# Kernel tuning notes

Measured on AMD Instinct MI355X. Metric: run time of the kernel, lower is better.

The kernel has to match this reference:

```python
import jax, jax.numpy as jnp
import numpy as np


def _gcn_conv(x, W, b, row, col, norm, n_nodes):
    # x: [N, Fin]; W: [Fin, Fout]. PyG GCNConv: linear -> normalized gather/scatter-add -> +bias
    h = x @ W                                   # [N, Fout]
    msgs = h[row] * norm[:, None]               # [E+N, Fout] gather + scale
    out = jax.ops.segment_sum(msgs, col, num_segments=n_nodes)  # scatter-add
    return out + b


def _gcn_norm(edge_index, n_nodes):
    # add self-loops, then sym-normalize: deg^{-1/2}[row] * deg^{-1/2}[col]
    loops = jnp.arange(n_nodes, dtype=edge_index.dtype)
    row = jnp.concatenate([edge_index[0], loops])
    col = jnp.concatenate([edge_index[1], loops])
    ones = jnp.ones(row.shape[0], dtype=jnp.float32)
    deg = jax.ops.segment_sum(ones, col, num_segments=n_nodes)
    dinv = jnp.where(deg > 0, jax.lax.rsqrt(deg), 0.0)
    norm = dinv[row] * dinv[col]
    return row, col, norm


def setup_inputs() -> dict:
    key = jax.random.key(0)
    k1, k2, k3, k4 = jax.random.split(key, 4)
    N, E, F, H, C = 100000, 1600000, 256, 128, 40
    x = jax.random.normal(k1, (N, F), dtype=jnp.float32)
    edge_index = jax.random.randint(k2, (2, E), 0, N, dtype=jnp.int64)
    W1 = jax.random.normal(k3, (F, H), dtype=jnp.float32) * (1.0 / np.sqrt(F))
    b1 = jnp.zeros((H,), dtype=jnp.float32)
    W2 = jax.random.normal(k4, (H, C), dtype=jnp.float32) * (1.0 / np.sqrt(H))
    b2 = jnp.zeros((C,), dtype=jnp.float32)
    return {"x": x, "edge_index": edge_index, "W1": W1, "b1": b1, "W2": W2, "b2": b2}


def reference(x, edge_index, W1, b1, W2, b2):
    n_nodes = x.shape[0]
    row, col, norm = _gcn_norm(edge_index, n_nodes)
    h = _gcn_conv(x, W1, b1, row, col, norm, n_nodes)
    h = jax.nn.relu(h)
    # F.dropout in eval mode is identity (reference run deterministically)
    h = _gcn_conv(h, W2, b2, row, col, norm, n_nodes)
    return jax.nn.log_softmax(h, axis=1)
```

## Files before the change

### kernel.cpp

```cpp
#include <hip/hip_runtime.h>
#include <hip/hip_bf16.h>
#include <math.h>
#include <stdint.h>

typedef unsigned short u16;
typedef unsigned int u32;
typedef __attribute__((ext_vector_type(8))) short short8;
typedef __attribute__((ext_vector_type(4))) float f32x4;
typedef __attribute__((ext_vector_type(2))) float f32x2;

#define BN 256
#define NBMAX 400
#define EPB 4096
#define ST1 160
#define ST2 192

__device__ __forceinline__ u16 bfbits(float f) {
    __hip_bfloat16 h = __float2bfloat16(f);
    return *reinterpret_cast<u16*>(&h);
}
__device__ __forceinline__ float bflo(u32 v) { return __uint_as_float(v << 16); }
__device__ __forceinline__ float bfhi(u32 v) { return __uint_as_float(v & 0xffff0000u); }

template <bool HI>
__device__ __forceinline__ f32x2 fp8pair(u32 v) {
#if __has_builtin(__builtin_amdgcn_cvt_pk_f32_fp8)
    return __builtin_amdgcn_cvt_pk_f32_fp8(v, HI);
#else
    f32x2 r;
    r.x = __builtin_amdgcn_cvt_f32_fp8(v, HI ? 2 : 0);
    r.y = __builtin_amdgcn_cvt_f32_fp8(v, HI ? 3 : 1);
    return r;
#endif
}

__global__ __launch_bounds__(256) void k_cnt(const int* __restrict__ col,
                                             int* __restrict__ gcnt, int E, int n, int nb) {
    __shared__ int sh[NBMAX];
    const int t = threadIdx.x;
    for (int i = t; i < nb; i += 256) sh[i] = 0;
    __syncthreads();
    const int base = blockIdx.x * EPB;
#pragma unroll
    for (int j = 0; j < 16; ++j) {
        int e = base + j * 256 + t;
        if (e < E) {
            unsigned c = (unsigned)col[e];
            if (c < (unsigned)n) atomicAdd(&sh[c >> 8], 1);
        }
    }
    __syncthreads();
    for (int i = t; i < nb; i += 256)
        if (sh[i]) atomicAdd(&gcnt[i], sh[i]);
}

__global__ __launch_bounds__(512) void k_bscan(const int* __restrict__ gcnt,
                                               int* __restrict__ ebase, int* __restrict__ cursor,
                                               int* __restrict__ off, int nb, int n) {
    __shared__ int sh[512];
    const int t = threadIdx.x;
    int v = (t < nb) ? gcnt[t] : 0;
    sh[t] = v;
    __syncthreads();
    for (int d = 1; d < 512; d <<= 1) {
        int x = (t >= d) ? sh[t - d] : 0;
        __syncthreads();
        sh[t] += x;
        __syncthreads();
    }
    if (t < nb) {
        int excl = sh[t] - v;
        ebase[t] = excl;
        cursor[t] = excl;
    }
    if (t == 0) {
        ebase[nb] = sh[511];
        off[n] = sh[511] + n;
    }
}

__global__ __launch_bounds__(256) void k_scat(const int* __restrict__ ei,
                                              int* __restrict__ cursor,
                                              u32* __restrict__ staging, int E, int n, int nb) {
    __shared__ int cnt[NBMAX];
    __shared__ int cbase[NBMAX];
    const int t = threadIdx.x;
    for (int i = t; i < nb; i += 256) cnt[i] = 0;
    __syncthreads();
    const int base = blockIdx.x * EPB;
    int rr[16], cc[16], rk[16];
#pragma unroll
    for (int j = 0; j < 16; ++j) {
        int e = base + j * 256 + t;
        cc[j] = -1;
        if (e < E) {
            unsigned r = (unsigned)ei[e], c = (unsigned)ei[E + e];
            if (r < (unsigned)n && c < (unsigned)n) {
                rr[j] = (int)r;
                cc[j] = (int)c;
                rk[j] = atomicAdd(&cnt[c >> 8], 1);
            }
        }
    }
    __syncthreads();
    for (int i = t; i < nb; i += 256)
        if (cnt[i]) cbase[i] = atomicAdd(&cursor[i], cnt[i]);
    __syncthreads();
#pragma unroll
    for (int j = 0; j < 16; ++j) {
        if (cc[j] >= 0) {
            int b = cc[j] >> 8;
            staging[cbase[b] + rk[j]] = (u32)rr[j] | ((u32)(cc[j] & (BN - 1)) << 17);
        }
    }
}

__global__ __launch_bounds__(256) void k_build(const u32* __restrict__ staging,
                                               const int* __restrict__ ebase,
                                               int* __restrict__ csrs, int* __restrict__ off,
                                               float* __restrict__ dinv, int n) {
    __shared__ int sh[256];
    __shared__ int cur[256];
    const int t = threadIdx.x;
    const int b = blockIdx.x;
    const int e0 = ebase[b], e1 = ebase[b + 1];
    const int node0 = b * BN;
    const int nn = min(BN, n - node0);
    sh[t] = 0;
    __syncthreads();
    for (int i = e0 + t; i < e1; i += 256)
        atomicAdd(&sh[staging[i] >> 17], 1);
    __syncthreads();
    const int mycnt = sh[t];
    const int myval = (t < nn) ? mycnt + 1 : 0;
    sh[t] = myval;
    __syncthreads();
    for (int d = 1; d < 256; d <<= 1) {
        int x = (t >= d) ? sh[t - d] : 0;
        __syncthreads();
        sh[t] += x;
        __syncthreads();
    }
    const int excl = sh[t] - myval;
    const int csrbase = e0 + node0;
    if (t < nn) {
        int node = node0 + t;
        int o = csrbase + excl;
        off[node] = o;
        dinv[node] = rsqrtf((float)(mycnt + 1));
        csrs[o] = node;
        cur[t] = o + 1;
    }
    __syncthreads();
    for (int i = e0 + t; i < e1; i += 256) {
        u32 v = staging[i];
        int p = atomicAdd(&cur[v >> 17], 1);
        csrs[p] = (int)(v & 0x1FFFF);
    }
}

__global__ void k_w1bf(const float* __restrict__ w1, short* __restrict__ w1bf) {
    int i = blockIdx.x * 256 + threadIdx.x;
    int e = i & 7, l = (i >> 3) & 63, kt = (i >> 9) & 7, ct = i >> 12;
    int k = kt * 32 + (l >> 4) * 8 + e;
    int c = ct * 16 + (l & 15);
    w1bf[i] = (short)bfbits(w1[(size_t)k * 128 + c]);
}

__device__ __forceinline__ int sigma128(int col) {
    int a = col >> 6, c = (col >> 4) & 3, lr = col & 15;
    return (a << 6) + (lr << 2) + c;
}
__global__ void k_prep(const float* __restrict__ b1, const float* __restrict__ w2,
                       float* __restrict__ b1p, float* __restrict__ w2p) {
    int i = blockIdx.x * 256 + threadIdx.x;
    if (i < 128) b1p[sigma128(i)] = b1[i];
    int j = i - 128;
    if (j >= 0 && j < 128 * 40) {
        int col = j / 40, jj = j - col * 40;
        w2p[sigma128(col) * 40 + jj] = w2[j];
    }
}

__global__ __launch_bounds__(256) void k_gemm1(const float* __restrict__ x,
                                               const short* __restrict__ w1bf,
                                               u32* __restrict__ hbf8, int n) {
    const int tid = threadIdx.x;
    const int wv = tid >> 6, l = tid & 63;
    const int mrow = wv >> 1, mcol = wv & 1;
    const int lr = l & 15, kg = l >> 4;
    const int n0 = blockIdx.x * 64;

    const float* xp[2];
#pragma unroll
    for (int m = 0; m < 2; ++m) {
        int row = n0 + 32 * mrow + 16 * m + lr;
        if (row > n - 1) row = n - 1;
        xp[m] = x + (size_t)row * 256 + kg * 8;
    }
    const short* bbase = w1bf + ((size_t)(4 * mcol) * 8) * 64 * 8 + (size_t)l * 8;

    float4 xv[2][8][2];
#pragma unroll
    for (int kt = 0; kt < 8; ++kt)
#pragma unroll
        for (int m = 0; m < 2; ++m) {
            xv[m][kt][0] = *(const float4*)(xp[m] + kt * 32);
            xv[m][kt][1] = *(const float4*)(xp[m] + kt * 32 + 4);
        }

    f32x4 zero = {0.f, 0.f, 0.f, 0.f};
    f32x4 acc[2][4];
#pragma unroll
    for (int m = 0; m < 2; ++m)
#pragma unroll
        for (int c = 0; c < 4; ++c) acc[m][c] = zero;

#pragma unroll
    for (int kt = 0; kt < 8; ++kt) {
        short8 af[2];
#pragma unroll
        for (int m = 0; m < 2; ++m) {
            float4 u = xv[m][kt][0];
            float4 v = xv[m][kt][1];
            short8 a;
            a[0] = (short)bfbits(u.x);
            a[1] = (short)bfbits(u.y);
            a[2] = (short)bfbits(u.z);
            a[3] = (short)bfbits(u.w);
            a[4] = (short)bfbits(v.x);
            a[5] = (short)bfbits(v.y);
            a[6] = (short)bfbits(v.z);
            a[7] = (short)bfbits(v.w);
            af[m] = a;
        }
#pragma unroll
        for (int c = 0; c < 4; ++c) {
            short8 bfrag = *(const short8*)(bbase + ((size_t)(c * 8 + kt) * 64) * 8);
#pragma unroll
            for (int m = 0; m < 2; ++m)
                acc[m][c] = __builtin_amdgcn_mfma_f32_16x16x32_bf16(af[m], bfrag,
                                                                    acc[m][c], 0, 0, 0);
        }
    }

#pragma unroll
    for (int m = 0; m < 2; ++m) {
        int rbase = n0 + 32 * mrow + 16 * m + kg * 4;
#pragma unroll
        for (int r = 0; r < 4; ++r) {
            int row = rbase + r;
            if (row < n) {
                int w = __builtin_amdgcn_cvt_pk_fp8_f32(acc[m][0][r], acc[m][1][r], 0, false);
                w = __builtin_amdgcn_cvt_pk_fp8_f32(acc[m][2][r], acc[m][3][r], w, true);
                hbf8[(size_t)row * 32 + 16 * mcol + lr] = (u32)w;
            }
        }
    }
}

__global__ __launch_bounds__(256) void k_agg1(const u32* __restrict__ hbf8,
                                              const int* __restrict__ off,
                                              const int* __restrict__ csrs,
                                              const float* __restrict__ dinv,
                                              const float* __restrict__ b1p,
                                              u16* __restrict__ h1b, int n) {
    __shared__ int s_s[8][ST1];
    __shared__ float s_f[8][ST1];
    const int t = threadIdx.x, h = t >> 5, fl = t & 31;
    const int node = blockIdx.x * 8 + h;
    const int nd = node < n ? node : n - 1;
    const float dn = dinv[nd];
    const int e0 = off[nd], e1 = off[nd + 1];
    const int deg = e1 - e0;
    const int nst = deg < ST1 ? deg : ST1;
    for (int i = fl; i < nst; i += 32) {
        int s = csrs[e0 + i];
        s_s[h][i] = s;
        s_f[h][i] = dinv[s] * dn;
    }
    __syncthreads();

    const int onst = __shfl_xor(nst, 32, 64);
    const int nmin = nst < onst ? nst : onst;
    const int nmax = nst > onst ? nst : onst;
    const int odeg = __shfl_xor(deg, 32, 64);
    const int dmax = deg > odeg ? deg : odeg;

    const u32* hb = hbf8;
    float a0 = 0.f, a1 = 0.f, a2 = 0.f, a3 = 0.f;
    int i = 0;
    for (; i + 4 <= nmin; i += 4) {
        int s0 = s_s[h][i], s1 = s_s[h][i + 1], s2 = s_s[h][i + 2], s3 = s_s[h][i + 3];
        float w0 = s_f[h][i], w1 = s_f[h][i + 1], w2v = s_f[h][i + 2], w3 = s_f[h][i + 3];
        u32 v0 = hb[(size_t)s0 * 32 + fl];
        u32 v1 = hb[(size_t)s1 * 32 + fl];
        u32 v2 = hb[(size_t)s2 * 32 + fl];
        u32 v3 = hb[(size_t)s3 * 32 + fl];
        f32x2 lo, hi;
        lo = fp8pair<false>(v0); hi = fp8pair<true>(v0);
        a0 = fmaf(lo.x, w0, a0); a1 = fmaf(lo.y, w0, a1);
        a2 = fmaf(hi.x, w0, a2); a3 = fmaf(hi.y, w0, a3);
        lo = fp8pair<false>(v1); hi = fp8pair<true>(v1);
        a0 = fmaf(lo.x, w1, a0); a1 = fmaf(lo.y, w1, a1);
        a2 = fmaf(hi.x, w1, a2); a3 = fmaf(hi.y, w1, a3);
        lo = fp8pair<false>(v2); hi = fp8pair<true>(v2);
        a0 = fmaf(lo.x, w2v, a0); a1 = fmaf(lo.y, w2v, a1);
        a2 = fmaf(hi.x, w2v, a2); a3 = fmaf(hi.y, w2v, a3);
        lo = fp8pair<false>(v3); hi = fp8pair<true>(v3);
        a0 = fmaf(lo.x, w3, a0); a1 = fmaf(lo.y, w3, a1);
        a2 = fmaf(hi.x, w3, a2); a3 = fmaf(hi.y, w3, a3);
    }
    for (; i < nmin; ++i) {
        int s = s_s[h][i];
        float w = s_f[h][i];
        u32 v = hb[(size_t)s * 32 + fl];
        f32x2 lo = fp8pair<false>(v), hi = fp8pair<true>(v);
        a0 = fmaf(lo.x, w, a0); a1 = fmaf(lo.y, w, a1);
        a2 = fmaf(hi.x, w, a2); a3 = fmaf(hi.y, w, a3);
    }
    for (; i < nmax; ++i) {
        bool ok = i < nst;
        int s = ok ? s_s[h][i] : nd;
        float w = ok ? s_f[h][i] : 0.f;
        u32 v = hb[(size_t)s * 32 + fl];
        f32x2 lo = fp8pair<false>(v), hi = fp8pair<true>(v);
        a0 = fmaf(lo.x, w, a0); a1 = fmaf(lo.y, w, a1);
        a2 = fmaf(hi.x, w, a2); a3 = fmaf(hi.y, w, a3);
    }
    for (int j = ST1; j < dmax; ++j) {
        bool ok = j < deg;
        int s = ok ? csrs[e0 + j] : nd;
        float w = ok ? dinv[s] * dn : 0.f;
        u32 v = hb[(size_t)s * 32 + fl];
        f32x2 lo = fp8pair<false>(v), hi = fp8pair<true>(v);
        a0 = fmaf(lo.x, w, a0); a1 = fmaf(lo.y, w, a1);
        a2 = fmaf(hi.x, w, a2); a3 = fmaf(hi.y, w, a3);
    }

    float4 bb = *(const float4*)(b1p + 4 * fl);
    float r0 = fmaxf(a0 + bb.x, 0.f);
    float r1 = fmaxf(a1 + bb.y, 0.f);
    float r2 = fmaxf(a2 + bb.z, 0.f);
    float r3 = fmaxf(a3 + bb.w, 0.f);
    if (node < n) {
        uint2 o;
        o.x = (u32)bfbits(r0) | ((u32)bfbits(r1) << 16);
        o.y = (u32)bfbits(r2) | ((u32)bfbits(r3) << 16);
        ((uint2*)h1b)[(size_t)node * 32 + fl] = o;
    }
}

__global__ __launch_bounds__(64) void k_gemm2(const u16* __restrict__ h1b,
                                              const float* __restrict__ w2p,
                                              u16* __restrict__ h2, int n) {
    __shared__ float hs[64 * 132];
    const int t = threadIdx.x;
    const int n0 = blockIdx.x * 64;
    const uint4* src = (const uint4*)(h1b + (size_t)n0 * 128);
#pragma unroll
    for (int i = 0; i < 16; ++i) {
        int idx = i * 64 + t;
        int r = idx >> 4, q = idx & 15;
        uint4 v = make_uint4(0u, 0u, 0u, 0u);
        if (n0 + r < n) v = src[(size_t)r * 16 + q];
        *(float4*)&hs[r * 132 + q * 8] =
            make_float4(bflo(v.x), bfhi(v.x), bflo(v.y), bfhi(v.y));
        *(float4*)&hs[r * 132 + q * 8 + 4] =
            make_float4(bflo(v.z), bfhi(v.z), bflo(v.w), bfhi(v.w));
    }
    __syncthreads();

    float acc[40];
#pragma unroll
    for (int c = 0; c < 40; ++c) acc[c] = 0.f;

    for (int k4 = 0; k4 < 32; ++k4) {
        float4 hv = *(const float4*)&hs[t * 132 + 4 * k4];
#pragma unroll
        for (int j = 0; j < 4; ++j) {
            float xv = (j == 0) ? hv.x : (j == 1) ? hv.y : (j == 2) ? hv.z : hv.w;
            const float* wr = w2p + (size_t)(4 * k4 + j) * 40;
#pragma unroll
            for (int c = 0; c < 40; ++c) acc[c] = fmaf(xv, wr[c], acc[c]);
        }
    }
    __syncthreads();
    u16* hsu = (u16*)&hs[0];
#pragma unroll
    for (int c = 0; c < 40; ++c) hsu[t * 40 + c] = bfbits(acc[c]);
    __syncthreads();
    const int lim = (n - n0 < 64 ? n - n0 : 64) * 40;
    u16* dst = h2 + (size_t)n0 * 40;
#pragma unroll
    for (int i = 0; i < 10; ++i) {
        int idx4 = i * 64 + t;
        if (idx4 * 4 < lim) {
            ushort4 v = ((const ushort4*)hsu)[idx4];
            *(ushort4*)(dst + idx4 * 4) = v;
        }
    }
}

__global__ __launch_bounds__(256) void k_agg2(const u16* __restrict__ h2,
                                              const int* __restrict__ off,
                                              const int* __restrict__ csrs,
                                              const float* __restrict__ dinv,
                                              const float* __restrict__ b2,
                                              float* __restrict__ out, int n) {
    __shared__ int s_s[4][ST2];
    __shared__ float s_f[4][ST2];
    const int t = threadIdx.x, wv = t >> 6, l = t & 63;
    const int node = blockIdx.x * 4 + wv;
    const int nd = node < n ? node : n - 1;
    const float dn = dinv[nd];
    const int e0 = off[nd], e1 = off[nd + 1];
    const int deg = e1 - e0;
    const int nst = deg < ST2 ? deg : ST2;
    for (int i = l; i < nst; i += 64) {
        int s = csrs[e0 + i];
        s_s[wv][i] = s;
        s_f[wv][i] = dinv[s] * dn;
    }
    __syncthreads();

    const int g = (l >= 40) ? 2 : (l >= 20 ? 1 : 0);
    int fl = l - 20 * g;
    if (fl > 19) fl = 19;
    const u32* hb = (const u32*)h2;

    float a0 = 0.f, a1 = 0.f;
    int base = 0;
    for (; base + 12 <= nst; base += 12) {
        int eA = base + g, eB = base + 3 + g, eC = base + 6 + g, eD = base + 9 + g;
        int sA = s_s[wv][eA], sB = s_s[wv][eB], sC = s_s[wv][eC], sD = s_s[wv][eD];
        float wA = s_f[wv][eA], wB = s_f[wv][eB], wC = s_f[wv][eC], wD = s_f[wv][eD];
        u32 vA = hb[(size_t)sA * 20 + fl];
        u32 vB = hb[(size_t)sB * 20 + fl];
        u32 vC = hb[(size_t)sC * 20 + fl];
        u32 vD = hb[(size_t)sD * 20 + fl];
        a0 = fmaf(bflo(vA), wA, a0); a1 = fmaf(bfhi(vA), wA, a1);
        a0 = fmaf(bflo(vB), wB, a0); a1 = fmaf(bfhi(vB), wB, a1);
        a0 = fmaf(bflo(vC), wC, a0); a1 = fmaf(bfhi(vC), wC, a1);
        a0 = fmaf(bflo(vD), wD, a0); a1 = fmaf(bfhi(vD), wD, a1);
    }
    for (; base + 6 <= nst; base += 6) {
        int eA = base + g, eB = base + 3 + g;
        int sA = s_s[wv][eA], sB = s_s[wv][eB];
        float wA = s_f[wv][eA], wB = s_f[wv][eB];
        u32 vA = hb[(size_t)sA * 20 + fl];
        u32 vB = hb[(size_t)sB * 20 + fl];
        a0 = fmaf(bflo(vA), wA, a0); a1 = fmaf(bfhi(vA), wA, a1);
        a0 = fmaf(bflo(vB), wB, a0); a1 = fmaf(bfhi(vB), wB, a1);
    }
    for (; base < nst; base += 3) {
        int e = base + g;
        bool ok = e < nst;
        int s = ok ? s_s[wv][e] : nd;
        float w = ok ? s_f[wv][e] : 0.f;
        u32 v = hb[(size_t)s * 20 + fl];
        a0 = fmaf(bflo(v), w, a0); a1 = fmaf(bfhi(v), w, a1);
    }
    for (int j = nst; j < deg; j += 3) {
        int e = j + g;
        bool ok = e < deg;
        int s = ok ? csrs[e0 + e] : nd;
        float w = ok ? dinv[s] * dn : 0.f;
        u32 v = hb[(size_t)s * 20 + fl];
        a0 = fmaf(bflo(v), w, a0); a1 = fmaf(bfhi(v), w, a1);
    }

    float p0 = __shfl(a0, (l + 20) & 63, 64);
    float q0 = __shfl(a0, (l + 40) & 63, 64);
    float p1 = __shfl(a1, (l + 20) & 63, 64);
    float q1 = __shfl(a1, (l + 40) & 63, 64);
    float2 bb = *(const float2*)(b2 + 2 * fl);
    float v0 = a0 + p0 + q0 + bb.x;
    float v1 = a1 + p1 + q1 + bb.y;

    const bool act = (l < 20);
    float m = act ? fmaxf(v0, v1) : -INFINITY;
#pragma unroll
    for (int d = 16; d > 0; d >>= 1) m = fmaxf(m, __shfl_xor(m, d, 32));
    float s = act ? (__expf(v0 - m) + __expf(v1 - m)) : 0.f;
#pragma unroll
    for (int d = 16; d > 0; d >>= 1) s += __shfl_xor(s, d, 32);
    float ls = logf(s);
    if (node < n && act) {
        float2 o = make_float2(v0 - m - ls, v1 - m - ls);
        *(float2*)(out + (size_t)node * 40 + 2 * fl) = o;
    }
}

extern "C" void kernel_launch(void* const* d_in, const int* in_sizes, int n_in,
                              void* d_out, int out_size, void* d_ws, size_t ws_size,
                              hipStream_t stream) {
    const float* x = (const float*)d_in[0];
    const int* ei = (const int*)d_in[1];
    const float* w1 = (const float*)d_in[2];
    const float* b1 = (const float*)d_in[3];
    const float* w2 = (const float*)d_in[4];
    const float* b2 = (const float*)d_in[5];
    float* out = (float*)d_out;

    const int N = in_sizes[0] / 256;
    const int E = in_sizes[1] / 2;
    const int NB = (N + BN - 1) / BN;

    char* p = (char*)d_ws;
    auto alloc = [&](size_t bytes) {
        char* r = p;
        p += (bytes + 255) & ~(size_t)255;
        return r;
    };
    int* gcnt = (int*)alloc((size_t)NB * 4);
    int* ebase = (int*)alloc((size_t)(NB + 1) * 4);
    int* cursor = (int*)alloc((size_t)NB * 4);
    int* off = (int*)alloc((size_t)(N + 1) * 4);
    float* dinv = (float*)alloc((size_t)N * 4);
    int* csrs = (int*)alloc((size_t)(E + N) * 4);
    short* w1bf = (short*)alloc(32768 * 2);
    float* b1p = (float*)alloc(128 * 4);
    float* w2p = (float*)alloc(128 * 40 * 4);
    u32* hbf8 = (u32*)alloc((size_t)N * 32 * 4);
    u16* h1b = (u16*)alloc((size_t)N * 128 * 2);
    u32* staging = (u32*)h1b;
    u16* h2 = (u16*)hbf8;

    const int nblk = (E + EPB - 1) / EPB;

    (void)hipMemsetAsync(gcnt, 0, (size_t)NB * 4, stream);
    k_cnt<<<nblk, 256, 0, stream>>>(ei + E, gcnt, E, N, NB);
    k_bscan<<<1, 512, 0, stream>>>(gcnt, ebase, cursor, off, NB, N);
    k_scat<<<nblk, 256, 0, stream>>>(ei, cursor, staging, E, N, NB);
    k_build<<<NB, 256, 0, stream>>>(staging, ebase, csrs, off, dinv, N);
    k_w1bf<<<128, 256, 0, stream>>>(w1, w1bf);
    k_prep<<<21, 256, 0, stream>>>(b1, w2, b1p, w2p);
    k_gemm1<<<(N + 63) / 64, 256, 0, stream>>>(x, w1bf, hbf8, N);
    k_agg1<<<(N + 7) / 8, 256, 0, stream>>>(hbf8, off, csrs, dinv, b1p, h1b, N);
    k_gemm2<<<(N + 63) / 64, 64, 0, stream>>>(h1b, w2p, h2, N);
    k_agg2<<<(N + 3) / 4, 256, 0, stream>>>(h2, off, csrs, dinv, b2, out, N);
}
```

Before: 253.1 us.

## Fuse setup kernels, overlap GEMM1 with edge scatter, quantize layer-2 features to int8

Merges the column-count, W1 conversion and bias/W2 permutation kernels into one launch, and runs the edge scatter and the first GEMM as separate block ranges of a single launch so they overlap. The layer-1 gather loop is unrolled to 8 independent loads. Layer-2 features are now stored as per-row-scaled int8 (16 words per row) instead of bf16, cutting gather bytes in the second aggregation, which is rewritten to process 4 channels per lane with 6 edge groups. The int8 quantization adds precision loss, and the fused launches add branching and can raise register pressure.

```diff
diff --git a/kernel.cpp b/kernel.cpp
--- a/kernel.cpp
+++ b/kernel.cpp
@@ -34,24 +34,50 @@
 #endif
 }
 
-__global__ __launch_bounds__(256) void k_cnt(const int* __restrict__ col,
-                                             int* __restrict__ gcnt, int E, int n, int nb) {
+__device__ __forceinline__ int sigma128(int col) {
+    int a = col >> 6, c = (col >> 4) & 3, lr = col & 15;
+    return (a << 6) + (lr << 2) + c;
+}
+
+__global__ __launch_bounds__(256) void k_pre(const int* __restrict__ ei, int E, int n, int nb,
+                                             int nblkc, int* __restrict__ gcnt,
+                                             const float* __restrict__ w1, short* __restrict__ w1bf,
+                                             const float* __restrict__ b1, const float* __restrict__ w2,
+                                             float* __restrict__ b1p, float* __restrict__ w2p) {
     __shared__ int sh[NBMAX];
     const int t = threadIdx.x;
-    for (int i = t; i < nb; i += 256) sh[i] = 0;
-    __syncthreads();
-    const int base = blockIdx.x * EPB;
-#pragma unroll
-    for (int j = 0; j < 16; ++j) {
-        int e = base + j * 256 + t;
-        if (e < E) {
-            unsigned c = (unsigned)col[e];
-            if (c < (unsigned)n) atomicAdd(&sh[c >> 8], 1);
-        }
-    }
-    __syncthreads();
-    for (int i = t; i < nb; i += 256)
-        if (sh[i]) atomicAdd(&gcnt[i], sh[i]);
+    const int b = blockIdx.x;
+    if (b < nblkc) {
+        const int* col = ei + E;
+        for (int i = t; i < nb; i += 256) sh[i] = 0;
+        __syncthreads();
+        const int base = b * EPB;
+#pragma unroll
+        for (int j = 0; j < 16; ++j) {
+            int e = base + j * 256 + t;
+            if (e < E) {
+                unsigned c = (unsigned)col[e];
+                if (c < (unsigned)n) atomicAdd(&sh[c >> 8], 1);
+            }
+        }
+        __syncthreads();
+        for (int i = t; i < nb; i += 256)
+            if (sh[i]) atomicAdd(&gcnt[i], sh[i]);
+    } else if (b < nblkc + 128) {
+        int i = (b - nblkc) * 256 + t;
+        int e = i & 7, l = (i >> 3) & 63, kt = (i >> 9) & 7, ct = i >> 12;
+        int k = kt * 32 + (l >> 4) * 8 + e;
+        int c = ct * 16 + (l & 15);
+        w1bf[i] = (short)bfbits(w1[(size_t)k * 128 + c]);
+    } else {
+        int i = (b - nblkc - 128) * 256 + t;
+        if (i < 128) b1p[sigma128(i)] = b1[i];
+        int j = i - 128;
+        if (j >= 0 && j < 128 * 40) {
+            int col = j / 40, jj = j - col * 40;
+            w2p[sigma128(col) * 40 + jj] = w2[j];
+        }
+    }
 }
 
 __global__ __launch_bounds__(512) void k_bscan(const int* __restrict__ gcnt,
@@ -79,117 +105,51 @@
     }
 }
 
-__global__ __launch_bounds__(256) void k_scat(const int* __restrict__ ei,
-                                              int* __restrict__ cursor,
-                                              u32* __restrict__ staging, int E, int n, int nb) {
+__global__ __launch_bounds__(256) void k_scatg1(const int* __restrict__ ei,
+                                                int* __restrict__ cursor, u32* __restrict__ staging,
+                                                int E, int n, int nb, int nblks,
+                                                const float* __restrict__ x,
+                                                const short* __restrict__ w1bf,
+                                                u32* __restrict__ hbf8) {
     __shared__ int cnt[NBMAX];
     __shared__ int cbase[NBMAX];
     const int t = threadIdx.x;
-    for (int i = t; i < nb; i += 256) cnt[i] = 0;
-    __syncthreads();
-    const int base = blockIdx.x * EPB;
-    int rr[16], cc[16], rk[16];
-#pragma unroll
-    for (int j = 0; j < 16; ++j) {
-        int e = base + j * 256 + t;
-        cc[j] = -1;
-        if (e < E) {
-            unsigned r = (unsigned)ei[e], c = (unsigned)ei[E + e];
-            if (r < (unsigned)n && c < (unsigned)n) {
-                rr[j] = (int)r;
-                cc[j] = (int)c;
-                rk[j] = atomicAdd(&cnt[c >> 8], 1);
+    if ((int)blockIdx.x < nblks) {
+        for (int i = t; i < nb; i += 256) cnt[i] = 0;
+        __syncthreads();
+        const int base = blockIdx.x * EPB;
+        int rr[16], cc[16], rk[16];
+#pragma unroll
+        for (int j = 0; j < 16; ++j) {
+            int e = base + j * 256 + t;
+            cc[j] = -1;
+            if (e < E) {
+                unsigned r = (unsigned)ei[e], c = (unsigned)ei[E + e];
+                if (r < (unsigned)n && c < (unsigned)n) {
+                    rr[j] = (int)r;
+                    cc[j] = (int)c;
+                    rk[j] = atomicAdd(&cnt[c >> 8], 1);
+                }
             }
         }
-    }
-    __syncthreads();
-    for (int i = t; i < nb; i += 256)
-        if (cnt[i]) cbase[i] = atomicAdd(&cursor[i], cnt[i]);
-    __syncthreads();
-#pragma unroll
-    for (int j = 0; j < 16; ++j) {
-        if (cc[j] >= 0) {
-            int b = cc[j] >> 8;
-            staging[cbase[b] + rk[j]] = (u32)rr[j] | ((u32)(cc[j] & (BN - 1)) << 17);
-        }
-    }
-}
-
-__global__ __launch_bounds__(256) void k_build(const u32* __restrict__ staging,
-                                               const int* __restrict__ ebase,
-                                               int* __restrict__ csrs, int* __restrict__ off,
-                                               float* __restrict__ dinv, int n) {
-    __shared__ int sh[256];
-    __shared__ int cur[256];
-    const int t = threadIdx.x;
-    const int b = blockIdx.x;
-    const int e0 = ebase[b], e1 = ebase[b + 1];
-    const int node0 = b * BN;
-    const int nn = min(BN, n - node0);
-    sh[t] = 0;
-    __syncthreads();
-    for (int i = e0 + t; i < e1; i += 256)
-        atomicAdd(&sh[staging[i] >> 17], 1);
-    __syncthreads();
-    const int mycnt = sh[t];
-    const int myval = (t < nn) ? mycnt + 1 : 0;
-    sh[t] = myval;
-    __syncthreads();
-    for (int d = 1; d < 256; d <<= 1) {
-        int x = (t >= d) ? sh[t - d] : 0;
-        __syncthreads();
-        sh[t] += x;
-        __syncthreads();
-    }
-    const int excl = sh[t] - myval;
-    const int csrbase = e0 + node0;
-    if (t < nn) {
-        int node = node0 + t;
-        int o = csrbase + excl;
-        off[node] = o;
-        dinv[node] = rsqrtf((float)(mycnt + 1));
-        csrs[o] = node;
-        cur[t] = o + 1;
-    }
-    __syncthreads();
-    for (int i = e0 + t; i < e1; i += 256) {
-        u32 v = staging[i];
-        int p = atomicAdd(&cur[v >> 17], 1);
-        csrs[p] = (int)(v & 0x1FFFF);
-    }
-}
-
-__global__ void k_w1bf(const float* __restrict__ w1, short* __restrict__ w1bf) {
-    int i = blockIdx.x * 256 + threadIdx.x;
-    int e = i & 7, l = (i >> 3) & 63, kt = (i >> 9) & 7, ct = i >> 12;
-    int k = kt * 32 + (l >> 4) * 8 + e;
-    int c = ct * 16 + (l & 15);
-    w1bf[i] = (short)bfbits(w1[(size_t)k * 128 + c]);
-}
-
-__device__ __forceinline__ int sigma128(int col) {
-    int a = col >> 6, c = (col >> 4) & 3, lr = col & 15;
-    return (a << 6) + (lr << 2) + c;
-}
-__global__ void k_prep(const float* __restrict__ b1, const float* __restrict__ w2,
-                       float* __restrict__ b1p, float* __restrict__ w2p) {
-    int i = blockIdx.x * 256 + threadIdx.x;
-    if (i < 128) b1p[sigma128(i)] = b1[i];
-    int j = i - 128;
-    if (j >= 0 && j < 128 * 40) {
-        int col = j / 40, jj = j - col * 40;
-        w2p[sigma128(col) * 40 + jj] = w2[j];
-    }
-}
-
-__global__ __launch_bounds__(256) void k_gemm1(const float* __restrict__ x,
-                                               const short* __restrict__ w1bf,
-                                               u32* __restrict__ hbf8, int n) {
-    const int tid = threadIdx.x;
-    const int wv = tid >> 6, l = tid & 63;
+        __syncthreads();
+        for (int i = t; i < nb; i += 256)
+            if (cnt[i]) cbase[i] = atomicAdd(&cursor[i], cnt[i]);
+        __syncthreads();
+#pragma unroll
+        for (int j = 0; j < 16; ++j) {
+            if (cc[j] >= 0) {
+                int b = cc[j] >> 8;
+                staging[cbase[b] + rk[j]] = (u32)rr[j] | ((u32)(cc[j] & (BN - 1)) << 17);
+            }
+        }
+        return;
+    }
+    const int bid = blockIdx.x - nblks;
+    const int wv = t >> 6, l = t & 63;
     const int mrow = wv >> 1, mcol = wv & 1;
     const int lr = l & 15, kg = l >> 4;
-    const int n0 = blockIdx.x * 64;
+    const int n0 = bid * 64;
 
     const float* xp[2];
 #pragma unroll
@@ -256,6 +216,50 @@
                 hbf8[(size_t)row * 32 + 16 * mcol + lr] = (u32)w;
             }
         }
+    }
+}
+
+__global__ __launch_bounds__(256) void k_build(const u32* __restrict__ staging,
+                                               const int* __restrict__ ebase,
+                                               int* __restrict__ csrs, int* __restrict__ off,
+                                               float* __restrict__ dinv, int n) {
+    __shared__ int sh[256];
+    __shared__ int cur[256];
+    const int t = threadIdx.x;
+    const int b = blockIdx.x;
+    const int e0 = ebase[b], e1 = ebase[b + 1];
+    const int node0 = b * BN;
+    const int nn = min(BN, n - node0);
+    sh[t] = 0;
+    __syncthreads();
+    for (int i = e0 + t; i < e1; i += 256)
+        atomicAdd(&sh[staging[i] >> 17], 1);
+    __syncthreads();
+    const int mycnt = sh[t];
+    const int myval = (t < nn) ? mycnt + 1 : 0;
+    sh[t] = myval;
+    __syncthreads();
+    for (int d = 1; d < 256; d <<= 1) {
+        int x = (t >= d) ? sh[t - d] : 0;
+        __syncthreads();
+        sh[t] += x;
+        __syncthreads();
+    }
+    const int excl = sh[t] - myval;
+    const int csrbase = e0 + node0;
+    if (t < nn) {
+        int node = node0 + t;
+        int o = csrbase + excl;
+        off[node] = o;
+        dinv[node] = rsqrtf((float)(mycnt + 1));
+        csrs[o] = node;
+        cur[t] = o + 1;
+    }
+    __syncthreads();
+    for (int i = e0 + t; i < e1; i += 256) {
+        u32 v = staging[i];
+        int p = atomicAdd(&cur[v >> 17], 1);
+        csrs[p] = (int)(v & 0x1FFFF);
     }
 }
 
@@ -290,26 +294,21 @@
     const u32* hb = hbf8;
     float a0 = 0.f, a1 = 0.f, a2 = 0.f, a3 = 0.f;
     int i = 0;
-    for (; i + 4 <= nmin; i += 4) {
-        int s0 = s_s[h][i], s1 = s_s[h][i + 1], s2 = s_s[h][i + 2], s3 = s_s[h][i + 3];
-        float w0 = s_f[h][i], w1 = s_f[h][i + 1], w2v = s_f[h][i + 2], w3 = s_f[h][i + 3];
-        u32 v0 = hb[(size_t)s0 * 32 + fl];
-        u32 v1 = hb[(size_t)s1 * 32 + fl];
-        u32 v2 = hb[(size_t)s2 * 32 + fl];
-        u32 v3 = hb[(size_t)s3 * 32 + fl];
-        f32x2 lo, hi;
-        lo = fp8pair<false>(v0); hi = fp8pair<true>(v0);
-        a0 = fmaf(lo.x, w0, a0); a1 = fmaf(lo.y, w0, a1);
-        a2 = fmaf(hi.x, w0, a2); a3 = fmaf(hi.y, w0, a3);
-        lo = fp8pair<false>(v1); hi = fp8pair<true>(v1);
-        a0 = fmaf(lo.x, w1, a0); a1 = fmaf(lo.y, w1, a1);
-        a2 = fmaf(hi.x, w1, a2); a3 = fmaf(hi.y, w1, a3);
-        lo = fp8pair<false>(v2); hi = fp8pair<true>(v2);
-        a0 = fmaf(lo.x, w2v, a0); a1 = fmaf(lo.y, w2v, a1);
-        a2 = fmaf(hi.x, w2v, a2); a3 = fmaf(hi.y, w2v, a3);
-        lo = fp8pair<false>(v3); hi = fp8pair<true>(v3);
-        a0 = fmaf(lo.x, w3, a0); a1 = fmaf(lo.y, w3, a1);
-        a2 = fmaf(hi.x, w3, a2); a3 = fmaf(hi.y, w3, a3);
+    for (; i + 8 <= nmin; i += 8) {
+        u32 vv[8];
+        float ww[8];
+#pragma unroll
+        for (int k = 0; k < 8; ++k) {
+            int s = s_s[h][i + k];
+            ww[k] = s_f[h][i + k];
+            vv[k] = hb[(size_t)s * 32 + fl];
+        }
+#pragma unroll
+        for (int k = 0; k < 8; ++k) {
+            f32x2 lo = fp8pair<false>(vv[k]), hi = fp8pair<true>(vv[k]);
+            a0 = fmaf(lo.x, ww[k], a0); a1 = fmaf(lo.y, ww[k], a1);
+            a2 = fmaf(hi.x, ww[k], a2); a3 = fmaf(hi.y, ww[k], a3);
+        }
     }
     for (; i < nmin; ++i) {
         int s = s_s[h][i];
@@ -353,7 +352,8 @@
 
 __global__ __launch_bounds__(64) void k_gemm2(const u16* __restrict__ h1b,
                                               const float* __restrict__ w2p,
-                                              u16* __restrict__ h2, int n) {
+                                              u32* __restrict__ h2q, float* __restrict__ scl,
+                                              int n) {
     __shared__ float hs[64 * 132];
     const int t = threadIdx.x;
     const int n0 = blockIdx.x * 64;
@@ -386,23 +386,39 @@
         }
     }
     __syncthreads();
-    u16* hsu = (u16*)&hs[0];
-#pragma unroll
-    for (int c = 0; c < 40; ++c) hsu[t * 40 + c] = bfbits(acc[c]);
-    __syncthreads();
-    const int lim = (n - n0 < 64 ? n - n0 : 64) * 40;
-    u16* dst = h2 + (size_t)n0 * 40;
-#pragma unroll
-    for (int i = 0; i < 10; ++i) {
-        int idx4 = i * 64 + t;
-        if (idx4 * 4 < lim) {
-            ushort4 v = ((const ushort4*)hsu)[idx4];
-            *(ushort4*)(dst + idx4 * 4) = v;
-        }
-    }
-}
-
-__global__ __launch_bounds__(256) void k_agg2(const u16* __restrict__ h2,
+
+    float mx = 0.f;
+#pragma unroll
+    for (int c = 0; c < 40; ++c) mx = fmaxf(mx, fabsf(acc[c]));
+    const float qs = mx > 0.f ? 127.f / mx : 0.f;
+    u32* rowp = (u32*)hs + t * 16;
+#pragma unroll
+    for (int j = 0; j < 10; ++j) {
+        u32 w = 0;
+#pragma unroll
+        for (int k = 0; k < 4; ++k) {
+            int q = __float2int_rn(acc[4 * j + k] * qs);
+            q = q > 127 ? 127 : (q < -127 ? -127 : q);
+            w |= ((u32)(q & 255)) << (8 * k);
+        }
+        rowp[j] = w;
+    }
+#pragma unroll
+    for (int j = 10; j < 16; ++j) rowp[j] = 0;
+    __syncthreads();
+    const int nrow = (n - n0 < 64) ? n - n0 : 64;
+    uint4* dst = (uint4*)(h2q + (size_t)n0 * 16);
+    const uint4* s4 = (const uint4*)hs;
+#pragma unroll
+    for (int i = 0; i < 4; ++i) {
+        int idx = i * 64 + t;
+        if ((idx >> 2) < nrow) dst[idx] = s4[idx];
+    }
+    if (t < nrow) scl[n0 + t] = mx * (1.f / 127.f);
+}
+
+__global__ __launch_bounds__(256) void k_agg2(const u32* __restrict__ h2q,
+                                              const float* __restrict__ scl,
                                               const int* __restrict__ off,
                                               const int* __restrict__ csrs,
                                               const float* __restrict__ dinv,
@@ -420,75 +436,85 @@
     for (int i = l; i < nst; i += 64) {
         int s = csrs[e0 + i];
         s_s[wv][i] = s;
-        s_f[wv][i] = dinv[s] * dn;
-    }
-    __syncthreads();
-
-    const int g = (l >= 40) ? 2 : (l >= 20 ? 1 : 0);
-    int fl = l - 20 * g;
-    if (fl > 19) fl = 19;
-    const u32* hb = (const u32*)h2;
-
-    float a0 = 0.f, a1 = 0.f;
+        s_f[wv][i] = dinv[s] * dn * scl[s];
+    }
+    __syncthreads();
+
+    int g = l / 10;
+    if (g > 5) g = 5;
+    const int fl = l - 10 * g;
+
+#define ACC4(v, w)                                                         \
+    {                                                                      \
+        a0 = fmaf((float)(int)(signed char)((v) & 0xff), (w), a0);         \
+        a1 = fmaf((float)(int)(signed char)(((v) >> 8) & 0xff), (w), a1);  \
+        a2 = fmaf((float)(int)(signed char)(((v) >> 16) & 0xff), (w), a2); \
+        a3 = fmaf((float)(int)(signed char)((v) >> 24), (w), a3);          \
+    }
+
+    float a0 = 0.f, a1 = 0.f, a2 = 0.f, a3 = 0.f;
     int base = 0;
-    for (; base + 12 <= nst; base += 12) {
-        int eA = base + g, eB = base + 3 + g, eC = base + 6 + g, eD = base + 9 + g;
+    for (; base + 24 <= nst; base += 24) {
+        int eA = base + g, eB = base + 6 + g, eC = base + 12 + g, eD = base + 18 + g;
         int sA = s_s[wv][eA], sB = s_s[wv][eB], sC = s_s[wv][eC], sD = s_s[wv][eD];
         float wA = s_f[wv][eA], wB = s_f[wv][eB], wC = s_f[wv][eC], wD = s_f[wv][eD];
-        u32 vA = hb[(size_t)sA * 20 + fl];
-        u32 vB = hb[(size_t)sB * 20 + fl];
-        u32 vC = hb[(size_t)sC * 20 + fl];
-        u32 vD = hb[(size_t)sD * 20 + fl];
-        a0 = fmaf(bflo(vA), wA, a0); a1 = fmaf(bfhi(vA), wA, a1);
-        a0 = fmaf(bflo(vB), wB, a0); a1 = fmaf(bfhi(vB), wB, a1);
-        a0 = fmaf(bflo(vC), wC, a0); a1 = fmaf(bfhi(vC), wC, a1);
-        a0 = fmaf(bflo(vD), wD, a0); a1 = fmaf(bfhi(vD), wD, a1);
-    }
-    for (; base + 6 <= nst; base += 6) {
-        int eA = base + g, eB = base + 3 + g;
+        u32 vA = h2q[(size_t)sA * 16 + fl];
+        u32 vB = h2q[(size_t)sB * 16 + fl];
+        u32 vC = h2q[(size_t)sC * 16 + fl];
+        u32 vD = h2q[(size_t)sD * 16 + fl];
+        ACC4(vA, wA); ACC4(vB, wB); ACC4(vC, wC); ACC4(vD, wD);
+    }
+    for (; base + 12 <= nst; base += 12) {
+        int eA = base + g, eB = base + 6 + g;
         int sA = s_s[wv][eA], sB = s_s[wv][eB];
         float wA = s_f[wv][eA], wB = s_f[wv][eB];
-        u32 vA = hb[(size_t)sA * 20 + fl];
-        u32 vB = hb[(size_t)sB * 20 + fl];
-        a0 = fmaf(bflo(vA), wA, a0); a1 = fmaf(bfhi(vA), wA, a1);
-        a0 = fmaf(bflo(vB), wB, a0); a1 = fmaf(bfhi(vB), wB, a1);
-    }
-    for (; base < nst; base += 3) {
+        u32 vA = h2q[(size_t)sA * 16 + fl];
+        u32 vB = h2q[(size_t)sB * 16 + fl];
+        ACC4(vA, wA); ACC4(vB, wB);
+    }
+    for (; base < nst; base += 6) {
         int e = base + g;
         bool ok = e < nst;
         int s = ok ? s_s[wv][e] : nd;
         float w = ok ? s_f[wv][e] : 0.f;
-        u32 v = hb[(size_t)s * 20 + fl];
-        a0 = fmaf(bflo(v), w, a0); a1 = fmaf(bfhi(v), w, a1);
-    }
-    for (int j = nst; j < deg; j += 3) {
+        u32 v = h2q[(size_t)s * 16 + fl];
+        ACC4(v, w);
+    }
+    for (int j = nst; j < deg; j += 6) {
         int e = j + g;
         bool ok = e < deg;
         int s = ok ? csrs[e0 + e] : nd;
-        float w = ok ? dinv[s] * dn : 0.f;
-        u32 v = hb[(size_t)s * 20 + fl];
-        a0 = fmaf(bflo(v), w, a0); a1 = fmaf(bfhi(v), w, a1);
-    }
-
-    float p0 = __shfl(a0, (l + 20) & 63, 64);
-    float q0 = __shfl(a0, (l + 40) & 63, 64);
-    float p1 = __shfl(a1, (l + 20) & 63, 64);
-    float q1 = __shfl(a1, (l + 40) & 63, 64);
-    float2 bb = *(const float2*)(b2 + 2 * fl);
-    float v0 = a0 + p0 + q0 + bb.x;
-    float v1 = a1 + p1 + q1 + bb.y;
-
-    const bool act = (l < 20);
-    float m = act ? fmaxf(v0, v1) : -INFINITY;
-#pragma unroll
-    for (int d = 16; d > 0; d >>= 1) m = fmaxf(m, __shfl_xor(m, d, 32));
-    float s = act ? (__expf(v0 - m) + __expf(v1 - m)) : 0.f;
-#pragma unroll
-    for (int d = 16; d > 0; d >>= 1) s += __shfl_xor(s, d, 32);
+        float w = ok ? dinv[s] * dn * scl[s] : 0.f;
+        u32 v = h2q[(size_t)s * 16 + fl];
+        ACC4(v, w);
+    }
+#undef ACC4
+
+    float t0 = __shfl(a0, (l + 30) & 63, 64);
+    float t1 = __shfl(a1, (l + 30) & 63, 64);
+    float t2 = __shfl(a2, (l + 30) & 63, 64);
+    float t3 = __shfl(a3, (l + 30) & 63, 64);
+    a0 += t0; a1 += t1; a2 += t2; a3 += t3;
+    float p0 = __shfl(a0, (l + 10) & 63, 64), q0 = __shfl(a0, (l + 20) & 63, 64);
+    float p1 = __shfl(a1, (l + 10) & 63, 64), q1 = __shfl(a1, (l + 20) & 63, 64);
+    float p2 = __shfl(a2, (l + 10) & 63, 64), q2 = __shfl(a2, (l + 20) & 63, 64);
+    float p3 = __shfl(a3, (l + 10) & 63, 64), q3 = __shfl(a3, (l + 20) & 63, 64);
+    a0 += p0 + q0; a1 += p1 + q1; a2 += p2 + q2; a3 += p3 + q3;
+
+    const bool act = (l < 10);
+    float4 bb = *(const float4*)(b2 + 4 * (act ? l : 9));
+    float v0 = a0 + bb.x, v1 = a1 + bb.y, v2 = a2 + bb.z, v3 = a3 + bb.w;
+
+    float m = act ? fmaxf(fmaxf(v0, v1), fmaxf(v2, v3)) : -INFINITY;
+#pragma unroll
+    for (int d = 8; d > 0; d >>= 1) m = fmaxf(m, __shfl_xor(m, d, 16));
+    float s = act ? (__expf(v0 - m) + __expf(v1 - m) + __expf(v2 - m) + __expf(v3 - m)) : 0.f;
+#pragma unroll
+    for (int d = 8; d > 0; d >>= 1) s += __shfl_xor(s, d, 16);
     float ls = logf(s);
     if (node < n && act) {
-        float2 o = make_float2(v0 - m - ls, v1 - m - ls);
-        *(float2*)(out + (size_t)node * 40 + 2 * fl) = o;
+        float4 o = make_float4(v0 - m - ls, v1 - m - ls, v2 - m - ls, v3 - m - ls);
+        *(float4*)(out + (size_t)node * 40 + 4 * l) = o;
     }
 }
 
@@ -518,6 +544,7 @@
     int* cursor = (int*)alloc((size_t)NB * 4);
     int* off = (int*)alloc((size_t)(N + 1) * 4);
     float* dinv = (float*)alloc((size_t)N * 4);
+    float* scl = (float*)alloc((size_t)N * 4);
     int* csrs = (int*)alloc((size_t)(E + N) * 4);
     short* w1bf = (short*)alloc(32768 * 2);
     float* b1p = (float*)alloc(128 * 4);
@@ -525,19 +552,19 @@
     u32* hbf8 = (u32*)alloc((size_t)N * 32 * 4);
     u16* h1b = (u16*)alloc((size_t)N * 128 * 2);
     u32* staging = (u32*)h1b;
-    u16* h2 = (u16*)hbf8;
+    u32* h2q = hbf8;
 
     const int nblk = (E + EPB - 1) / EPB;
+    const int g1blk = (N + 63) / 64;
 
     (void)hipMemsetAsync(gcnt, 0, (size_t)NB * 4, stream);
-    k_cnt<<<nblk, 256, 0, stream>>>(ei + E, gcnt, E, N, NB);
+    k_pre<<<nblk + 128 + 21, 256, 0, stream>>>(ei, E, N, NB, nblk, gcnt, w1, w1bf,
+                                               b1, w2, b1p, w2p);
     k_bscan<<<1, 512, 0, stream>>>(gcnt, ebase, cursor, off, NB, N);
-    k_scat<<<nblk, 256, 0, stream>>>(ei, cursor, staging, E, N, NB);
+    k_scatg1<<<nblk + g1blk, 256, 0, stream>>>(ei, cursor, staging, E, N, NB, nblk,
+                                               x, w1bf, hbf8);
     k_build<<<NB, 256, 0, stream>>>(staging, ebase, csrs, off, dinv, N);
-    k_w1bf<<<128, 256, 0, stream>>>(w1, w1bf);
-    k_prep<<<21, 256, 0, stream>>>(b1, w2, b1p, w2p);
-    k_gemm1<<<(N + 63) / 64, 256, 0, stream>>>(x, w1bf, hbf8, N);
     k_agg1<<<(N + 7) / 8, 256, 0, stream>>>(hbf8, off, csrs, dinv, b1p, h1b, N);
-    k_gemm2<<<(N + 63) / 64, 64, 0, stream>>>(h1b, w2p, h2, N);
-    k_agg2<<<(N + 3) / 4, 256, 0, stream>>>(h2, off, csrs, dinv, b2, out, N);
-}
+    k_gemm2<<<g1blk, 64, 0, stream>>>(h1b, w2p, h2q, scl, N);
+    k_agg2<<<(N + 3) / 4, 256, 0, stream>>>(h2q, scl, off, csrs, dinv, b2, out, N);
+}
```

Result: faster. 240.5 us (-5.0%).
